# Kernel optimization log

Hardware: AMD Instinct MI355X
Metric: run time of the kernel (lower is better)

## Reference

```python
import jax, jax.numpy as jnp
import numpy as np


def setup_inputs() -> dict:
    key = jax.random.key(0)
    k1, k2, k3, k4 = jax.random.split(key, 4)
    B, S, d_in, d_out = 4, 2048, 1024, 1024
    x = jax.random.normal(k1, (B, S, d_in), dtype=jnp.float32)
    # weights stored as [d_in, d_out] (transpose of torch Linear weight), scaled like default init
    scale = 1.0 / np.sqrt(d_in)
    Wq = jax.random.normal(k2, (d_in, d_out), dtype=jnp.float32) * scale
    Wk = jax.random.normal(k3, (d_in, d_out), dtype=jnp.float32) * scale
    Wv = jax.random.normal(k4, (d_in, d_out), dtype=jnp.float32) * scale
    return {"x": x, "Wq": Wq, "Wk": Wk, "Wv": Wv}


def reference(x, Wq, Wk, Wv):
    # x: [B, S, d_in]; projections: [B, S, d_out]
    q = jnp.einsum("bsd,de->bse", x, Wq)
    k = jnp.einsum("bsd,de->bse", x, Wk)
    v = jnp.einsum("bsd,de->bse", x, Wv)
    d_out = k.shape[-1]
    # full S x S scores (naive, as in original)
    scores = jnp.einsum("bqe,bke->bqk", q, k)
    # NOTE: original applies softmax over ALL keys first, then multiplies by
    # a lower-triangular causal mask WITHOUT renormalizing. Reproduce exactly.
    weights = jax.nn.softmax(scores / jnp.sqrt(jnp.float32(d_out)), axis=-1)
    S = scores.shape[1]
    mask = jnp.tril(jnp.ones((S, S), dtype=weights.dtype))
    masked = weights * mask  # [B, S, S]
    context = jnp.einsum("bqk,bke->bqe", masked, v)
    return context
```

## Files before the change

### kernel.cpp

```cpp
#include <hip/hip_runtime.h>
#include <hip/hip_bf16.h>
#include <hip/hip_fp16.h>

typedef __attribute__((ext_vector_type(8))) short bf16x8;
typedef __attribute__((ext_vector_type(4))) float f32x4;

__device__ __forceinline__ unsigned short f2bf(float f) {
    unsigned u = __float_as_uint(f);
    u += 0x7fffu + ((u >> 16) & 1u);
    return (unsigned short)(u >> 16);
}
__device__ __forceinline__ float bf2f(unsigned short b) {
    return __uint_as_float(((unsigned)b) << 16);
}

#define GLOAD_LDS16(g, l)                                                           \
    __builtin_amdgcn_global_load_lds(                                               \
        (const __attribute__((address_space(1))) void*)(g),                         \
        (__attribute__((address_space(3))) void*)(l), 16, 0, 0)

#define TBM 256
#define TBN 256
#define TBK 64

template <int OMODE>
__global__ __launch_bounds__(512, 2) void gemm256(
    const unsigned short* __restrict__ A, const unsigned short* __restrict__ B,
    void* __restrict__ Cv, float* __restrict__ Zb, int M, int N, int K,
    long long sA, long long sB, long long sC) {
    __shared__ unsigned short lds[2][4][128 * 64];

    const int bz = blockIdx.z;
    A += (size_t)bz * (size_t)sA;
    B += (size_t)bz * (size_t)sB;

    const int bm = blockIdx.x, bn = blockIdx.y;
    const int tid = threadIdx.x;
    const int wid = tid >> 6, lane = tid & 63;
    const int wr = wid >> 2, wc = wid & 3;
    const int frow = lane & 15, kgrp = lane >> 4;
    const int nt = K / TBK;

    const unsigned short* Abase = A + (size_t)(bm * TBM) * K;
    const unsigned short* Bbase = B + (size_t)(bn * TBN) * K;

    auto STAGE_H = [&](const unsigned short* gtb, int kt, unsigned short* dsthalf) {
#pragma unroll
        for (int ld = 0; ld < 2; ++ld) {
            const int c = tid + ld * 512;
            const int row = c >> 3, c8 = c & 7;
            GLOAD_LDS16(gtb + (size_t)row * K + kt * TBK + ((c8 ^ (row & 7)) << 3),
                        (char*)dsthalf + ld * 8192 + wid * 1024);
        }
    };

    f32x4 acc[8][4];
#pragma unroll
    for (int i = 0; i < 8; ++i)
#pragma unroll
        for (int j = 0; j < 4; ++j) acc[i][j] = (f32x4){0.f, 0.f, 0.f, 0.f};

    STAGE_H(Bbase, 0, &lds[0][2][0]);
    STAGE_H(Bbase + 128 * (size_t)K, 0, &lds[0][3][0]);
    STAGE_H(Abase, 0, &lds[0][0][0]);
    STAGE_H(Abase + 128 * (size_t)K, 0, &lds[0][1][0]);

    for (int t = 0; t < nt; ++t) {
        const int buf = t & 1, bufN = buf ^ 1;
        const unsigned short* Ah = &lds[buf][wr][0];
        const unsigned short* Bh = &lds[buf][2 + (wc >> 1)][0];

        if (t + 1 < nt) {
            STAGE_H(Bbase, t + 1, &lds[bufN][2][0]);
            STAGE_H(Bbase + 128 * (size_t)K, t + 1, &lds[bufN][3][0]);
            asm volatile("s_waitcnt vmcnt(4)" ::: "memory");
        } else {
            asm volatile("s_waitcnt vmcnt(0)" ::: "memory");
        }
        __builtin_amdgcn_s_barrier();

        bf16x8 bfrag[4][2];
#pragma unroll
        for (int n = 0; n < 4; ++n) {
            const int rB = (wc & 1) * 64 + n * 16 + frow;
            const int sw = (rB & 7) << 3;
#pragma unroll
            for (int kk = 0; kk < 2; ++kk)
                bfrag[n][kk] =
                    *(const bf16x8*)&Bh[rB * 64 + ((((kk << 2) + kgrp) << 3) ^ sw)];
        }
        {
            bf16x8 afrag[2][2];
#pragma unroll
            for (int m2 = 0; m2 < 2; ++m2) {
                const int rA = m2 * 16 + frow;
                const int sw = (rA & 7) << 3;
#pragma unroll
                for (int kk = 0; kk < 2; ++kk)
                    afrag[m2][kk] =
                        *(const bf16x8*)&Ah[rA * 64 + ((((kk << 2) + kgrp) << 3) ^ sw)];
            }
            __builtin_amdgcn_s_setprio(1);
#pragma unroll
            for (int m2 = 0; m2 < 2; ++m2)
#pragma unroll
                for (int n = 0; n < 4; ++n)
#pragma unroll
                    for (int kk = 0; kk < 2; ++kk)
                        acc[m2][n] = __builtin_amdgcn_mfma_f32_16x16x32_bf16(
                            afrag[m2][kk], bfrag[n][kk], acc[m2][n], 0, 0, 0);
            __builtin_amdgcn_s_setprio(0);
        }

#pragma unroll
        for (int q = 1; q < 4; ++q) {
            if (q == 1 && t + 1 < nt) STAGE_H(Abase, t + 1, &lds[bufN][0][0]);
            if (q == 2 && t + 1 < nt)
                STAGE_H(Abase + 128 * (size_t)K, t + 1, &lds[bufN][1][0]);
            bf16x8 afrag[2][2];
#pragma unroll
            for (int m2 = 0; m2 < 2; ++m2) {
                const int rA = q * 32 + m2 * 16 + frow;
                const int sw = (rA & 7) << 3;
#pragma unroll
                for (int kk = 0; kk < 2; ++kk)
                    afrag[m2][kk] =
                        *(const bf16x8*)&Ah[rA * 64 + ((((kk << 2) + kgrp) << 3) ^ sw)];
            }
            __builtin_amdgcn_s_setprio(1);
#pragma unroll
            for (int m2 = 0; m2 < 2; ++m2)
#pragma unroll
                for (int n = 0; n < 4; ++n)
#pragma unroll
                    for (int kk = 0; kk < 2; ++kk)
                        acc[q * 2 + m2][n] = __builtin_amdgcn_mfma_f32_16x16x32_bf16(
                            afrag[m2][kk], bfrag[n][kk], acc[q * 2 + m2][n], 0, 0, 0);
            __builtin_amdgcn_s_setprio(0);
        }
    }

    const size_t row0 = (size_t)bm * TBM + wr * 128 + kgrp * 4;
    const int col0 = bn * TBN + wc * 64 + frow;
    if (OMODE == 0) {
        unsigned short* Cp = (unsigned short*)Cv + (size_t)bz * (size_t)sC;
#pragma unroll
        for (int mi = 0; mi < 8; ++mi)
#pragma unroll
            for (int rr = 0; rr < 4; ++rr) {
                unsigned short* op = Cp + (row0 + mi * 16 + rr) * N + col0;
#pragma unroll
                for (int n = 0; n < 4; ++n) op[n * 16] = f2bf(acc[mi][n][rr]);
            }
    } else {
        unsigned short* Cp = (unsigned short*)Cv + (size_t)bz * (size_t)sC;
        float rs[8][4];
#pragma unroll
        for (int mi = 0; mi < 8; ++mi)
#pragma unroll
            for (int rr = 0; rr < 4; ++rr) {
                const int rowg = (int)(row0 + mi * 16 + rr);
                unsigned short* op = Cp + (size_t)rowg * N + col0;
                float zsum = 0.f;
#pragma unroll
                for (int n = 0; n < 4; ++n) {
                    float e = __expf(acc[mi][n][rr] * 0.03125f);
                    unsigned short pb = f2bf(e);
                    zsum += bf2f(pb);
                    op[n * 16] = (col0 + n * 16 <= rowg) ? pb : (unsigned short)0;
                }
                rs[mi][rr] = zsum;
            }
#pragma unroll
        for (int mi = 0; mi < 8; ++mi)
#pragma unroll
            for (int rr = 0; rr < 4; ++rr) {
                float v = rs[mi][rr];
                v += __shfl_xor(v, 1);
                v += __shfl_xor(v, 2);
                v += __shfl_xor(v, 4);
                v += __shfl_xor(v, 8);
                rs[mi][rr] = v;
            }
        if (frow == 0) {
            float* Zr = Zb + (size_t)bz * M + row0;
#pragma unroll
            for (int mi = 0; mi < 8; ++mi)
#pragma unroll
                for (int rr = 0; rr < 4; ++rr)
                    atomicAdd(&Zr[mi * 16 + rr], rs[mi][rr]);
        }
    }
}

#define BM 128
#define BN 128
#define BK 32

__global__ __launch_bounds__(256) void gemm_pv(
    const unsigned short* __restrict__ A, const unsigned short* __restrict__ B,
    float* __restrict__ C, const float* __restrict__ Z, int M, int N, int K,
    long long sA, long long sB, long long sC) {
    __shared__ unsigned short As[2][BM * BK];
    __shared__ unsigned short Bs[2][BN * BK];

    const int bz = blockIdx.z;
    A += (size_t)bz * (size_t)sA;
    B += (size_t)bz * (size_t)sB;

    const int bm = gridDim.x - 1 - blockIdx.x;
    const int bn = blockIdx.y;
    const int tid = threadIdx.x;
    const int wid = tid >> 6;
    const int lane = tid & 63;
    const int wr = wid >> 1, wc = wid & 1;
    const int frow = lane & 15;
    const int kgrp = lane >> 4;

    int nt = K / BK;
    {
        int lim = (bm + 1) * (BM / BK);
        if (lim < nt) nt = lim;
    }

    const int c0 = (wid * 2 + 0) * 64 + lane;
    const int c1 = (wid * 2 + 1) * 64 + lane;
    const unsigned short* Abase = A + (size_t)(bm * BM) * K;
    const unsigned short* Bbase = B + (size_t)(bn * BN) * K;

    auto STAGE = [&](int kt, int buf) {
        const unsigned short* Ag = Abase + kt * BK;
        const unsigned short* Bg = Bbase + kt * BK;
        GLOAD_LDS16(Ag + (size_t)(c0 >> 2) * K + (c0 & 3) * 8,
                    (char*)&As[buf][0] + (wid * 2 + 0) * 1024);
        GLOAD_LDS16(Bg + (size_t)(c0 >> 2) * K + (c0 & 3) * 8,
                    (char*)&Bs[buf][0] + (wid * 2 + 0) * 1024);
        GLOAD_LDS16(Ag + (size_t)(c1 >> 2) * K + (c1 & 3) * 8,
                    (char*)&As[buf][0] + (wid * 2 + 1) * 1024);
        GLOAD_LDS16(Bg + (size_t)(c1 >> 2) * K + (c1 & 3) * 8,
                    (char*)&Bs[buf][0] + (wid * 2 + 1) * 1024);
    };

    f32x4 acc[4][4];
#pragma unroll
    for (int mi = 0; mi < 4; ++mi)
#pragma unroll
        for (int ni = 0; ni < 4; ++ni) acc[mi][ni] = (f32x4){0.f, 0.f, 0.f, 0.f};

    STAGE(0, 0);
    __syncthreads();

    for (int kt = 0; kt < nt; ++kt) {
        const int buf = kt & 1;
        if (kt + 1 < nt) STAGE(kt + 1, buf ^ 1);
        bf16x8 af[4], bfr[4];
#pragma unroll
        for (int mi = 0; mi < 4; ++mi) {
            int row = wr * 64 + mi * 16 + frow;
            af[mi] = *(const bf16x8*)&As[buf][row * BK + kgrp * 8];
        }
#pragma unroll
        for (int ni = 0; ni < 4; ++ni) {
            int col = wc * 64 + ni * 16 + frow;
            bfr[ni] = *(const bf16x8*)&Bs[buf][col * BK + kgrp * 8];
        }
#pragma unroll
        for (int mi = 0; mi < 4; ++mi)
#pragma unroll
            for (int ni = 0; ni < 4; ++ni)
                acc[mi][ni] = __builtin_amdgcn_mfma_f32_16x16x32_bf16(
                    af[mi], bfr[ni], acc[mi][ni], 0, 0, 0);
        __syncthreads();
    }

    const size_t row0 = (size_t)bm * BM + wr * 64 + kgrp * 4;
    const int col0 = bn * BN + wc * 64 + frow;
    float* Cp = C + (size_t)bz * (size_t)sC;
    const float* Zp = Z + (size_t)bz * M;
#pragma unroll
    for (int mi = 0; mi < 4; ++mi)
#pragma unroll
        for (int r = 0; r < 4; ++r) {
            const float ri = 1.0f / Zp[row0 + mi * 16 + r];
            float* op = Cp + (row0 + mi * 16 + r) * N + col0;
#pragma unroll
            for (int ni = 0; ni < 4; ++ni) op[ni * 16] = acc[mi][ni][r] * ri;
        }
}

__global__ __launch_bounds__(256) void zero_f32(float* __restrict__ p, int n) {
    int i = blockIdx.x * blockDim.x + threadIdx.x;
    if (i < n) p[i] = 0.f;
}

__global__ __launch_bounds__(256) void cvt_f32_bf16(
    const float* __restrict__ in, unsigned short* __restrict__ out, int n) {
    int idx = blockIdx.x * blockDim.x + threadIdx.x;
    int stride = gridDim.x * blockDim.x;
    for (int i = idx * 4; i < n; i += stride * 4) {
        float4 v = *(const float4*)(in + i);
        ushort4 o;
        o.x = f2bf(v.x); o.y = f2bf(v.y); o.z = f2bf(v.z); o.w = f2bf(v.w);
        *(ushort4*)(out + i) = o;
    }
}

__global__ __launch_bounds__(256) void transpose_cvt_w(
    const float* __restrict__ in, unsigned short* __restrict__ out, int Kd, int Nd) {
    __shared__ float t[32][33];
    const int tr = blockIdx.y * 32, tc = blockIdx.x * 32;
    const int r = threadIdx.x >> 3, c4 = (threadIdx.x & 7) * 4;
    float4 v = *(const float4*)&in[(size_t)(tr + r) * Nd + tc + c4];
    t[r][c4 + 0] = v.x; t[r][c4 + 1] = v.y; t[r][c4 + 2] = v.z; t[r][c4 + 3] = v.w;
    __syncthreads();
    ushort4 o;
    o.x = f2bf(t[c4 + 0][r]); o.y = f2bf(t[c4 + 1][r]);
    o.z = f2bf(t[c4 + 2][r]); o.w = f2bf(t[c4 + 3][r]);
    *(ushort4*)&out[(size_t)(tc + r) * Kd + tr + c4] = o;
}

__global__ __launch_bounds__(256) void transpose_bf16(
    const unsigned short* __restrict__ in, unsigned short* __restrict__ out,
    int R, int Cc) {
    __shared__ unsigned short t[32][36];
    const int bz = blockIdx.z;
    in += (size_t)bz * R * Cc;
    out += (size_t)bz * R * Cc;
    const int tr = blockIdx.y * 32, tc = blockIdx.x * 32;
    const int r = threadIdx.x >> 3, c4 = (threadIdx.x & 7) * 4;
    ushort4 v = *(const ushort4*)&in[(size_t)(tr + r) * Cc + tc + c4];
    t[r][c4 + 0] = v.x; t[r][c4 + 1] = v.y; t[r][c4 + 2] = v.z; t[r][c4 + 3] = v.w;
    __syncthreads();
    ushort4 o;
    o.x = t[c4 + 0][r]; o.y = t[c4 + 1][r]; o.z = t[c4 + 2][r]; o.w = t[c4 + 3][r];
    *(ushort4*)&out[(size_t)(tc + r) * R + tr + c4] = o;
}

extern "C" void kernel_launch(void* const* d_in, const int* in_sizes, int n_in,
                              void* d_out, int out_size, void* d_ws, size_t ws_size,
                              hipStream_t stream) {
    const int B = 4, S = 2048, D = 1024;
    const size_t M = (size_t)B * S;

    const float* x = (const float*)d_in[0];
    float* out = (float*)d_out;

    unsigned short* xb = (unsigned short*)d_ws;
    unsigned short* Wt = xb + M * D;
    unsigned short* Qb = Wt + 3 * (size_t)D * D;
    unsigned short* Kb = Qb + M * D;
    unsigned short* Vb = Kb + M * D;
    unsigned short* Vt = Vb + M * D;
    unsigned short* Sc = Vt + M * D;
    float* Zd = (float*)(Sc + (size_t)B * S * S);
    const size_t need =
        (size_t)(M * D * 5 + 3 * (size_t)D * D + (size_t)B * S * S) * 2 +
        (size_t)B * S * 4;
    if (ws_size < need) return;

    zero_f32<<<(B * S + 255) / 256, 256, 0, stream>>>(Zd, B * S);
    cvt_f32_bf16<<<2048, 256, 0, stream>>>(x, xb, (int)(M * D));
    dim3 tg(D / 32, D / 32, 1);
    transpose_cvt_w<<<tg, 256, 0, stream>>>((const float*)d_in[1], Wt + 0 * (size_t)D * D, D, D);
    transpose_cvt_w<<<tg, 256, 0, stream>>>((const float*)d_in[2], Wt + 1 * (size_t)D * D, D, D);
    transpose_cvt_w<<<tg, 256, 0, stream>>>((const float*)d_in[3], Wt + 2 * (size_t)D * D, D, D);

    gemm256<0><<<dim3(M / TBM, D / TBN, 3), 512, 0, stream>>>(
        xb, Wt, (void*)Qb, nullptr, (int)M, D, D, 0LL, (long long)D * D,
        (long long)(M * D));

    transpose_bf16<<<dim3(D / 32, S / 32, B), 256, 0, stream>>>(Vb, Vt, S, D);

    gemm256<2><<<dim3(S / TBM, S / TBN, B), 512, 0, stream>>>(
        Qb, Kb, (void*)Sc, Zd, S, S, D, (long long)S * D, (long long)S * D,
        (long long)S * S);

    gemm_pv<<<dim3(S / BM, D / BN, B), 256, 0, stream>>>(
        Sc, Vt, out, Zd, S, D, S, (long long)S * S, (long long)D * S,
        (long long)S * D);
}
```

Before: 180.5 us.

## Restructure GEMM main loop into 8-wave ping-pong with B prefetched two tiles ahead

Reorganizes the bf16 MFMA GEMM k-loop so the B tile for iteration t+2 is prefetched into the current buffer while A for t+1 streams in. Each quarter-step gets a barrier before and after its MFMA block, in the style of ping-pong scheduling that interleaves wave groups' load and compute phases. The goal is deeper global-load latency hiding. In exchange it adds many more barriers per iteration. Overwriting the current B buffer relies on every wave having already read its B fragments into registers at q==0.

Result: slower. 187.5 us (+3.9%).

```diff
diff --git a/kernel.cpp b/kernel.cpp
--- a/kernel.cpp
+++ b/kernel.cpp
@@ -60,63 +60,38 @@
 #pragma unroll
         for (int j = 0; j < 4; ++j) acc[i][j] = (f32x4){0.f, 0.f, 0.f, 0.f};
 
+    STAGE_H(Abase, 0, &lds[0][0][0]);
+    STAGE_H(Abase + 128 * (size_t)K, 0, &lds[0][1][0]);
     STAGE_H(Bbase, 0, &lds[0][2][0]);
     STAGE_H(Bbase + 128 * (size_t)K, 0, &lds[0][3][0]);
-    STAGE_H(Abase, 0, &lds[0][0][0]);
-    STAGE_H(Abase + 128 * (size_t)K, 0, &lds[0][1][0]);
+    if (1 < nt) {
+        STAGE_H(Bbase, 1, &lds[1][2][0]);
+        STAGE_H(Bbase + 128 * (size_t)K, 1, &lds[1][3][0]);
+        asm volatile("s_waitcnt vmcnt(4)" ::: "memory");
+    } else {
+        asm volatile("s_waitcnt vmcnt(0)" ::: "memory");
+    }
+    __builtin_amdgcn_s_barrier();
 
     for (int t = 0; t < nt; ++t) {
         const int buf = t & 1, bufN = buf ^ 1;
         const unsigned short* Ah = &lds[buf][wr][0];
         const unsigned short* Bh = &lds[buf][2 + (wc >> 1)][0];
-
-        if (t + 1 < nt) {
-            STAGE_H(Bbase, t + 1, &lds[bufN][2][0]);
-            STAGE_H(Bbase + 128 * (size_t)K, t + 1, &lds[bufN][3][0]);
-            asm volatile("s_waitcnt vmcnt(4)" ::: "memory");
-        } else {
-            asm volatile("s_waitcnt vmcnt(0)" ::: "memory");
-        }
-        __builtin_amdgcn_s_barrier();
-
         bf16x8 bfrag[4][2];
-#pragma unroll
-        for (int n = 0; n < 4; ++n) {
-            const int rB = (wc & 1) * 64 + n * 16 + frow;
-            const int sw = (rB & 7) << 3;
-#pragma unroll
-            for (int kk = 0; kk < 2; ++kk)
-                bfrag[n][kk] =
-                    *(const bf16x8*)&Bh[rB * 64 + ((((kk << 2) + kgrp) << 3) ^ sw)];
-        }
-        {
-            bf16x8 afrag[2][2];
-#pragma unroll
-            for (int m2 = 0; m2 < 2; ++m2) {
-                const int rA = m2 * 16 + frow;
-                const int sw = (rA & 7) << 3;
-#pragma unroll
-                for (int kk = 0; kk < 2; ++kk)
-                    afrag[m2][kk] =
-                        *(const bf16x8*)&Ah[rA * 64 + ((((kk << 2) + kgrp) << 3) ^ sw)];
-            }
-            __builtin_amdgcn_s_setprio(1);
-#pragma unroll
-            for (int m2 = 0; m2 < 2; ++m2)
-#pragma unroll
-                for (int n = 0; n < 4; ++n)
+
+#pragma unroll
+        for (int q = 0; q < 4; ++q) {
+            if (q == 0) {
+#pragma unroll
+                for (int n = 0; n < 4; ++n) {
+                    const int rB = (wc & 1) * 64 + n * 16 + frow;
+                    const int sw = (rB & 7) << 3;
 #pragma unroll
                     for (int kk = 0; kk < 2; ++kk)
-                        acc[m2][n] = __builtin_amdgcn_mfma_f32_16x16x32_bf16(
-                            afrag[m2][kk], bfrag[n][kk], acc[m2][n], 0, 0, 0);
-            __builtin_amdgcn_s_setprio(0);
-        }
-
-#pragma unroll
-        for (int q = 1; q < 4; ++q) {
-            if (q == 1 && t + 1 < nt) STAGE_H(Abase, t + 1, &lds[bufN][0][0]);
-            if (q == 2 && t + 1 < nt)
-                STAGE_H(Abase + 128 * (size_t)K, t + 1, &lds[bufN][1][0]);
+                        bfrag[n][kk] = *(const bf16x8*)
+                            &Bh[rB * 64 + ((((kk << 2) + kgrp) << 3) ^ sw)];
+                }
+            }
             bf16x8 afrag[2][2];
 #pragma unroll
             for (int m2 = 0; m2 < 2; ++m2) {
@@ -124,9 +99,19 @@
                 const int sw = (rA & 7) << 3;
 #pragma unroll
                 for (int kk = 0; kk < 2; ++kk)
-                    afrag[m2][kk] =
-                        *(const bf16x8*)&Ah[rA * 64 + ((((kk << 2) + kgrp) << 3) ^ sw)];
-            }
+                    afrag[m2][kk] = *(const bf16x8*)
+                        &Ah[rA * 64 + ((((kk << 2) + kgrp) << 3) ^ sw)];
+            }
+
+            if (q == 0 && t + 1 < nt) STAGE_H(Abase, t + 1, &lds[bufN][0][0]);
+            if (q == 1 && t + 1 < nt)
+                STAGE_H(Abase + 128 * (size_t)K, t + 1, &lds[bufN][1][0]);
+            if (q == 2 && t + 2 < nt) STAGE_H(Bbase, t + 2, &lds[buf][2][0]);
+            if (q == 3 && t + 2 < nt)
+                STAGE_H(Bbase + 128 * (size_t)K, t + 2, &lds[buf][3][0]);
+
+            __builtin_amdgcn_s_barrier();
+
             __builtin_amdgcn_s_setprio(1);
 #pragma unroll
             for (int m2 = 0; m2 < 2; ++m2)
@@ -137,6 +122,15 @@
                         acc[q * 2 + m2][n] = __builtin_amdgcn_mfma_f32_16x16x32_bf16(
                             afrag[m2][kk], bfrag[n][kk], acc[q * 2 + m2][n], 0, 0, 0);
             __builtin_amdgcn_s_setprio(0);
+
+            if (q == 3) {
+                if (t + 2 < nt) {
+                    asm volatile("s_waitcnt vmcnt(4)" ::: "memory");
+                } else {
+                    asm volatile("s_waitcnt vmcnt(0)" ::: "memory");
+                }
+            }
+            __builtin_amdgcn_s_barrier();
         }
     }
 
```

## Fuse V transpose into projection GEMM epilogue and skip upper-triangle score stores

Applied to the files above, without the earlier changes.

The projection GEMM now writes the V slice straight into transposed layout through an LDS staging tile, so the separate transpose kernel and its extra read/write of V go away. The scores GEMM skips global stores for tiles entirely above the causal diagonal, since the PV kernel presumably never reads them. The LDS array grows to hold a 256x264 padded transpose tile, which may affect occupancy, and the skipped stores rely on the consumer ignoring those tiles.

Result: no change. 177.7 us (-1.5%).

```diff
diff --git a/kernel.cpp b/kernel.cpp
--- a/kernel.cpp
+++ b/kernel.cpp
@@ -3,6 +3,7 @@
 #include <hip/hip_fp16.h>
 
 typedef __attribute__((ext_vector_type(8))) short bf16x8;
+typedef __attribute__((ext_vector_type(8))) unsigned short u16x8;
 typedef __attribute__((ext_vector_type(4))) float f32x4;
 
 __device__ __forceinline__ unsigned short f2bf(float f) {
@@ -26,9 +27,12 @@
 template <int OMODE>
 __global__ __launch_bounds__(512, 2) void gemm256(
     const unsigned short* __restrict__ A, const unsigned short* __restrict__ B,
-    void* __restrict__ Cv, float* __restrict__ Zb, int M, int N, int K,
+    void* __restrict__ Cv, float* __restrict__ Zb,
+    unsigned short* __restrict__ VtOut, int M, int N, int K,
     long long sA, long long sB, long long sC) {
-    __shared__ unsigned short lds[2][4][128 * 64];
+    __shared__ unsigned short ldsraw[256 * 264];
+    typedef unsigned short LdsBuf[4][128 * 64];
+    LdsBuf* lds = (LdsBuf*)ldsraw;
 
     const int bz = blockIdx.z;
     A += (size_t)bz * (size_t)sA;
@@ -143,17 +147,41 @@
     const size_t row0 = (size_t)bm * TBM + wr * 128 + kgrp * 4;
     const int col0 = bn * TBN + wc * 64 + frow;
     if (OMODE == 0) {
-        unsigned short* Cp = (unsigned short*)Cv + (size_t)bz * (size_t)sC;
-#pragma unroll
-        for (int mi = 0; mi < 8; ++mi)
-#pragma unroll
-            for (int rr = 0; rr < 4; ++rr) {
-                unsigned short* op = Cp + (row0 + mi * 16 + rr) * N + col0;
-#pragma unroll
-                for (int n = 0; n < 4; ++n) op[n * 16] = f2bf(acc[mi][n][rr]);
-            }
+        if (VtOut != nullptr && bz == 2) {
+            __syncthreads();
+            unsigned short (*T)[264] = (unsigned short (*)[264])ldsraw;
+            const int rloc = wr * 128 + kgrp * 4;
+#pragma unroll
+            for (int mi = 0; mi < 8; ++mi)
+#pragma unroll
+                for (int rr = 0; rr < 4; ++rr)
+#pragma unroll
+                    for (int n = 0; n < 4; ++n)
+                        T[wc * 64 + n * 16 + frow][rloc + mi * 16 + rr] =
+                            f2bf(acc[mi][n][rr]);
+            __syncthreads();
+            const int c = tid >> 1, rh = (tid & 1) * 128;
+            const int b = bm >> 3;
+            const int srow0 = (bm & 7) * 256;
+            unsigned short* vp = VtOut +
+                ((size_t)b * N + (size_t)(bn * TBN + c)) * 2048 + srow0 + rh;
+#pragma unroll
+            for (int k = 0; k < 16; ++k)
+                *(u16x8*)(vp + k * 8) = *(const u16x8*)&T[c][rh + k * 8];
+        } else {
+            unsigned short* Cp = (unsigned short*)Cv + (size_t)bz * (size_t)sC;
+#pragma unroll
+            for (int mi = 0; mi < 8; ++mi)
+#pragma unroll
+                for (int rr = 0; rr < 4; ++rr) {
+                    unsigned short* op = Cp + (row0 + mi * 16 + rr) * N + col0;
+#pragma unroll
+                    for (int n = 0; n < 4; ++n) op[n * 16] = f2bf(acc[mi][n][rr]);
+                }
+        }
     } else {
         unsigned short* Cp = (unsigned short*)Cv + (size_t)bz * (size_t)sC;
+        const bool doStore = (bn <= bm);
         float rs[8][4];
 #pragma unroll
         for (int mi = 0; mi < 8; ++mi)
@@ -167,7 +195,8 @@
                     float e = __expf(acc[mi][n][rr] * 0.03125f);
                     unsigned short pb = f2bf(e);
                     zsum += bf2f(pb);
-                    op[n * 16] = (col0 + n * 16 <= rowg) ? pb : (unsigned short)0;
+                    if (doStore)
+                        op[n * 16] = (col0 + n * 16 <= rowg) ? pb : (unsigned short)0;
                 }
                 rs[mi][rr] = zsum;
             }
@@ -319,23 +348,6 @@
     *(ushort4*)&out[(size_t)(tc + r) * Kd + tr + c4] = o;
 }
 
-__global__ __launch_bounds__(256) void transpose_bf16(
-    const unsigned short* __restrict__ in, unsigned short* __restrict__ out,
-    int R, int Cc) {
-    __shared__ unsigned short t[32][36];
-    const int bz = blockIdx.z;
-    in += (size_t)bz * R * Cc;
-    out += (size_t)bz * R * Cc;
-    const int tr = blockIdx.y * 32, tc = blockIdx.x * 32;
-    const int r = threadIdx.x >> 3, c4 = (threadIdx.x & 7) * 4;
-    ushort4 v = *(const ushort4*)&in[(size_t)(tr + r) * Cc + tc + c4];
-    t[r][c4 + 0] = v.x; t[r][c4 + 1] = v.y; t[r][c4 + 2] = v.z; t[r][c4 + 3] = v.w;
-    __syncthreads();
-    ushort4 o;
-    o.x = t[c4 + 0][r]; o.y = t[c4 + 1][r]; o.z = t[c4 + 2][r]; o.w = t[c4 + 3][r];
-    *(ushort4*)&out[(size_t)(tc + r) * R + tr + c4] = o;
-}
-
 extern "C" void kernel_launch(void* const* d_in, const int* in_sizes, int n_in,
                               void* d_out, int out_size, void* d_ws, size_t ws_size,
                               hipStream_t stream) {
@@ -366,14 +378,12 @@
     transpose_cvt_w<<<tg, 256, 0, stream>>>((const float*)d_in[3], Wt + 2 * (size_t)D * D, D, D);
 
     gemm256<0><<<dim3(M / TBM, D / TBN, 3), 512, 0, stream>>>(
-        xb, Wt, (void*)Qb, nullptr, (int)M, D, D, 0LL, (long long)D * D,
+        xb, Wt, (void*)Qb, nullptr, Vt, (int)M, D, D, 0LL, (long long)D * D,
         (long long)(M * D));
 
-    transpose_bf16<<<dim3(D / 32, S / 32, B), 256, 0, stream>>>(Vb, Vt, S, D);
-
     gemm256<2><<<dim3(S / TBM, S / TBN, B), 512, 0, stream>>>(
-        Qb, Kb, (void*)Sc, Zd, S, S, D, (long long)S * D, (long long)S * D,
-        (long long)S * S);
+        Qb, Kb, (void*)Sc, Zd, nullptr, S, S, D, (long long)S * D,
+        (long long)S * D, (long long)S * S);
 
     gemm_pv<<<dim3(S / BM, D / BN, B), 256, 0, stream>>>(
         Sc, Vt, out, Zd, S, D, S, (long long)S * S, (long long)D * S,
```
